# Optimization experiments

Measured on AMD Instinct MI355X. Metric: run time of the kernel, lower is better.

## Reference

```python
import jax, jax.numpy as jnp
import numpy as np

SPLINE_ORDER = 3
BN_EPS = 1e-5


def make_grid(grid_size, lo=-1.0, hi=1.0):
    # torch KANLinear grid: uniform on [lo,hi] extended by spline_order knots each side
    h = (hi - lo) / grid_size
    return jnp.arange(-SPLINE_ORDER, grid_size + SPLINE_ORDER + 1, dtype=jnp.float32) * h + lo


def b_splines(x, grid, k=SPLINE_ORDER):
    # x: [...], grid: [G+2k+1] -> bases [..., G+k] (Cox-de Boor recursion)
    x = x[..., None]
    bases = ((x >= grid[:-1]) & (x < grid[1:])).astype(x.dtype)
    for j in range(1, k + 1):
        left = (x - grid[: -(j + 1)]) / (grid[j:-1] - grid[: -(j + 1)])
        right = (grid[j + 1:] - x) / (grid[j + 1:] - grid[1:-j])
        bases = left * bases[..., :-1] + right * bases[..., 1:]
    return bases


def extract_patches(x, d):
    # 3x3 dilated sliding windows, stride 1, padding == dilation -> same HxW
    B, C, H, W = x.shape
    xp = jnp.pad(x, ((0, 0), (0, 0), (d, d), (d, d)))
    pats = [xp[:, :, ki * d:ki * d + H, kj * d:kj * d + W]
            for ki in range(3) for kj in range(3)]
    return jnp.stack(pats, axis=-1)  # [B,C,H,W,9] (kh-major, matching torch Unfold)


def batchnorm(x, g, b):
    # training-mode BN (torch default forward): batch statistics, biased variance
    mean = x.mean(axis=(0, 2, 3), keepdims=True)
    var = x.var(axis=(0, 2, 3), keepdims=True)
    return (x - mean) / jnp.sqrt(var + BN_EPS) * g[None, :, None, None] + b[None, :, None, None]


def se_block(x, w1, w2):
    y = x.mean(axis=(2, 3))                                  # [B,C]
    y = jax.nn.sigmoid(jax.nn.relu(y @ w1.T) @ w2.T)         # [B,C]
    return x * y[:, :, None, None]


def kan_conv(x, base_w, spline_w, grid, dilation):
    # one KANLinear(9->1) per (out,in) channel pair, summed over in channels
    p = extract_patches(x, dilation)                          # [B,Ci,H,W,9]
    base = jnp.einsum('bihwk,oik->bohw', jax.nn.silu(p), base_w)
    bs = b_splines(p, grid)                                   # [B,Ci,H,W,9,G+k]
    spl = jnp.einsum('bihwkg,oikg->bohw', bs, spline_w)
    return base + spl


def kan_branch(x, base_w, spline_w, grid, dilation, bn_g, bn_b, se_w1, se_w2):
    y = kan_conv(x, base_w, spline_w, grid, dilation)
    y = jax.nn.relu(batchnorm(y, bn_g, bn_b))
    return se_block(y, se_w1, se_w2)


def setup_inputs() -> dict:
    key = jax.random.key(0)
    ks = jax.random.split(key, 16)
    B, Ci, Co, H, W = 2, 64, 64, 64, 64
    r = Co // 16
    d = {"x": jax.random.normal(ks[0], (B, Ci, H, W), jnp.float32)}
    for i, (bname, G) in enumerate([(6, 3), (12, 6), (18, 9)]):
        kk = jax.random.split(ks[1 + i], 4)
        d[f"base_w{bname}"] = jax.random.normal(kk[0], (Co, Ci, 9), jnp.float32) / np.sqrt(9.0 * Ci)
        d[f"spline_w{bname}"] = jax.random.normal(kk[1], (Co, Ci, 9, G + SPLINE_ORDER), jnp.float32) * (0.1 / np.sqrt(9.0 * Ci))
        d[f"bn{bname}_g"] = jnp.ones((Co,), jnp.float32)
        d[f"bn{bname}_b"] = jnp.zeros((Co,), jnp.float32)
        d[f"se{bname}_w1"] = jax.random.normal(kk[2], (r, Co), jnp.float32) / np.sqrt(Co)
        d[f"se{bname}_w2"] = jax.random.normal(kk[3], (Co, r), jnp.float32) / np.sqrt(r)
    d["gp_conv_w"] = jax.random.normal(ks[4], (Co, Ci), jnp.float32) / np.sqrt(Ci)
    d["gp_conv_b"] = jnp.zeros((Co,), jnp.float32)
    d["gp_bn_g"] = jnp.ones((Co,), jnp.float32)
    d["gp_bn_b"] = jnp.zeros((Co,), jnp.float32)
    d["gp_se_w1"] = jax.random.normal(ks[5], (r, Co), jnp.float32) / np.sqrt(Co)
    d["gp_se_w2"] = jax.random.normal(ks[6], (Co, r), jnp.float32) / np.sqrt(r)
    d["fuse_w"] = jax.random.normal(ks[7], (Co, 4 * Co), jnp.float32) / np.sqrt(4.0 * Co)
    d["fuse_b"] = jnp.zeros((Co,), jnp.float32)
    d["fuse_bn_g"] = jnp.ones((Co,), jnp.float32)
    d["fuse_bn_b"] = jnp.zeros((Co,), jnp.float32)
    return d


def reference(x, base_w6, spline_w6, bn6_g, bn6_b, se6_w1, se6_w2,
              base_w12, spline_w12, bn12_g, bn12_b, se12_w1, se12_w2,
              base_w18, spline_w18, bn18_g, bn18_b, se18_w1, se18_w2,
              gp_conv_w, gp_conv_b, gp_bn_g, gp_bn_b, gp_se_w1, gp_se_w2,
              fuse_w, fuse_b, fuse_bn_g, fuse_bn_b):
    B, Ci, H, W = x.shape
    # global-pool branch: avgpool -> 1x1 conv -> BN -> ReLU -> SE -> bilinear
    # upsample (1x1 source => pure broadcast, align_corners irrelevant)
    gp = x.mean(axis=(2, 3)) @ gp_conv_w.T + gp_conv_b      # [B,Co]
    gp = gp[:, :, None, None]
    gp = jax.nn.relu(batchnorm(gp, gp_bn_g, gp_bn_b))
    gp = se_block(gp, gp_se_w1, gp_se_w2)
    gp = jnp.broadcast_to(gp, (B, gp.shape[1], H, W))
    # KAN dilated branches
    b6 = kan_branch(x, base_w6, spline_w6, make_grid(3), 6, bn6_g, bn6_b, se6_w1, se6_w2)
    b12 = kan_branch(x, base_w12, spline_w12, make_grid(6), 12, bn12_g, bn12_b, se12_w1, se12_w2)
    b18 = kan_branch(x, base_w18, spline_w18, make_grid(9), 18, bn18_g, bn18_b, se18_w1, se18_w2)
    cat = jnp.concatenate([b6, b12, b18, gp], axis=1)        # [B,4Co,H,W]
    out = jnp.einsum('bihw,oi->bohw', cat, fuse_w) + fuse_b[None, :, None, None]
    out = jax.nn.relu(batchnorm(out, fuse_bn_g, fuse_bn_b))
    return out
```

## Files before the change

kernel.cpp:

```cpp
#include <hip/hip_runtime.h>
#include <hip/hip_bf16.h>
#include <math.h>

#define DEV __device__ __forceinline__

static constexpr int HW  = 4096;
static constexpr int POS = 8192;
static constexpr int SLAB = 6 * 64 * 4096;

typedef __attribute__((ext_vector_type(8)))  short short8;
typedef __attribute__((ext_vector_type(16))) float floatx16;
typedef __attribute__((ext_vector_type(4)))  unsigned int uint4v;

template<int G>
DEV void bsplines(float x, float* out ) {
  const float h = 2.0f / (float)G;
  float knot[G + 7];
#pragma unroll
  for (int t = 0; t < G + 7; ++t) knot[t] = -1.0f + (float)(t - 3) * h;
  float bb[G + 6];
#pragma unroll
  for (int t = 0; t < G + 6; ++t) bb[t] = (x >= knot[t] && x < knot[t + 1]) ? 1.0f : 0.0f;
#pragma unroll
  for (int j = 1; j <= 3; ++j) {
    const float inv = (float)G / (2.0f * (float)j);
#pragma unroll
    for (int t = 0; t < G + 6 - j; ++t) {
      float left  = (x - knot[t]) * inv;
      float right = (knot[t + j + 1] - x) * inv;
      bb[t] = left * bb[t] + right * bb[t + 1];
    }
  }
#pragma unroll
  for (int t = 0; t < G + 3; ++t) out[t] = bb[t];
}

DEV float sigmoidf_(float x) { return 1.0f / (1.0f + __expf(-x)); }

DEV float block_reduce_256(float v, float* sb) {
  __syncthreads();
#pragma unroll
  for (int off = 32; off > 0; off >>= 1) v += __shfl_down(v, off, 64);
  int lane = threadIdx.x & 63, wid = threadIdx.x >> 6;
  if (lane == 0) sb[wid] = v;
  __syncthreads();
  return sb[0] + sb[1] + sb[2] + sb[3];
}


template<int CF>
DEV void wprep_body(const float* __restrict__ base_w, const float* __restrict__ spline_w,
                    __hip_bfloat16* __restrict__ Wt, int bid) {
  constexpr int KC = 64 * CF;
  int lin = bid * 256 + threadIdx.x;
  int ic = lin % KC;
  int rest = lin / KC;
  int o = rest & 63, tap = rest >> 6;
  int c = ic % CF, i = ic / CF;
  float v = (c == 0) ? base_w[(o * 64 + i) * 9 + tap]
                     : spline_w[((o * 64 + i) * 9 + tap) * (CF - 1) + (c - 1)];
  int s = ic >> 4, kk = ic & 15, q = kk >> 3, r = kk & 7, hh = o >> 5;
  int l = q * 32 + (o & 31);
  Wt[(size_t)tap * (64 * KC) + s * 1024 + hh * 512 + l * 8 + r] = __float2bfloat16(v);
}

template<int G>
DEV void c0r_body(int ki, const float* __restrict__ sw, float* __restrict__ out,
                  float* shmem ) {
  constexpr int NB = G + 3;
  int o = threadIdx.x & 63, part = threadIdx.x >> 6;
  float b0[NB];
  bsplines<G>(0.0f, b0);
  float s = 0.0f;
  for (int kj = 0; kj < 3; ++kj) {
    int tap = ki * 3 + kj;
    for (int i = part * 16; i < part * 16 + 16; ++i) {
      const float* p = sw + ((size_t)(o * 64 + i) * 9 + tap) * NB;
#pragma unroll
      for (int c = 0; c < NB; ++c) s += p[c] * b0[c];
    }
  }
  shmem[part * 64 + o] = s;
  __syncthreads();
  if (part == 0)
    out[ki * 64 + o] = shmem[o] + shmem[64 + o] + shmem[128 + o] + shmem[192 + o];
}

template<int G, int D>
DEV void features_body(const float* __restrict__ x, __hip_bfloat16* __restrict__ F, int bid,
                       __hip_bfloat16* lds ) {
  constexpr int CF = G + 4;
  constexpr int NB = G + 3;
  constexpr int WP = 64 + 2 * D;
  constexpr int NG = WP / 4;
  constexpr int KC = 64 * CF;
  constexpr int RS = 64 * CF + 16;
  int ws = threadIdx.x & 3, i = threadIdx.x >> 2;
  int wpg = bid % NG;
  int rest = bid / NG;
  int h = rest & 63, b = rest >> 6;
  int wp = wpg * 4 + ws;
  int w = wp - D;
  float xv = (w >= 0 && w < 64) ? x[((size_t)(b * 64 + i) * 64 + h) * 64 + w] : 0.0f;
  float s = xv * sigmoidf_(xv);
  float bas[NB];
  bsplines<G>(xv, bas);
  __hip_bfloat16* dst = lds + ws * RS + i * CF;
  dst[0] = __float2bfloat16(s);
#pragma unroll
  for (int c = 1; c < CF; ++c) dst[c] = __float2bfloat16(bas[c - 1]);
  __syncthreads();
  constexpr int TOTV = 32 * CF;
  uint4v* g = (uint4v*)(F + (size_t)(b * 64 + h) * WP * KC);
  const uint4v* l = (const uint4v*)lds;
  for (int t = threadIdx.x; t < TOTV; t += 256) {
    int sc = t >> 3, r = t & 7, wl = r >> 1, k4 = r & 1;
    g[(size_t)(sc * WP + wpg * 4 + wl) * 2 + k4] = l[wl * (8 * CF + 2) + sc * 2 + k4];
  }
}

__global__ void prepfeat_k(const float* __restrict__ x,
                           __hip_bfloat16* F0, __hip_bfloat16* F1, __hip_bfloat16* F2,
                           const float* bw0, const float* sw0, const float* bw1,
                           const float* sw1, const float* bw2, const float* sw2,
                           __hip_bfloat16* W0, __hip_bfloat16* W1, __hip_bfloat16* W2,
                           float* C0r, const float* fuse_w, float* fwT,
                           float* xm, float* accz ) {
  __shared__ uint4v ldsq[424];
  __shared__ float shmem[256];
  __hip_bfloat16* lds = (__hip_bfloat16*)ldsq;
  int bid = blockIdx.x, tid = threadIdx.x;
  if (bid < 2432)      { features_body<3, 6>(x, F0, bid, lds); return; }
  else if (bid < 5248) { features_body<6, 12>(x, F1, bid - 2432, lds); return; }
  else if (bid < 8448) { features_body<9, 18>(x, F2, bid - 5248, lds); return; }
  int pb = bid - 8448;
  if (pb < 1008)      { wprep_body<7>(bw0, sw0, W0, pb); }
  else if (pb < 2448) { wprep_body<10>(bw1, sw1, W1, pb - 1008); }
  else if (pb < 4320) { wprep_body<13>(bw2, sw2, W2, pb - 2448); }
  else if (pb < 4329) {
    int idx = pb - 4320, br = idx / 3, ki = idx % 3;
    if (br == 0)      c0r_body<3>(ki, sw0, C0r, shmem);
    else if (br == 1) c0r_body<6>(ki, sw1, C0r + 192, shmem);
    else              c0r_body<9>(ki, sw2, C0r + 384, shmem);
  } else if (pb < 4377) {
    int lin = (pb - 4329) * 256 + tid;
    int o = lin & 63, i2 = lin >> 6;
    fwT[i2 * 64 + o] = fuse_w[o * 256 + i2];
  } else if (pb < 4505) {
    int bi = pb - 4377;
    const float* p = x + (size_t)bi * HW;
    float s = 0.0f;
    for (int t = tid; t < HW; t += 256) s += p[t];
    s = block_reduce_256(s, shmem);
    if (tid == 0) xm[bi] = s * (1.0f / HW);
  } else {
    for (int t = tid; t < 896; t += 256) accz[t] = 0.0f;
  }
}

DEV floatx16 mfma_bf16(short8 a, short8 b, floatx16 c) {
  return __builtin_amdgcn_mfma_f32_32x32x16_bf16(a, b, c, 0, 0, 0);
}

template<int CF, int DD>
DEV void conv_dev(int ki, int b, int hp, const short* __restrict__ F,
                  const short* __restrict__ W, const float* __restrict__ C0r,
                  float* __restrict__ ypart, int br, float* __restrict__ red) {
  constexpr int KC = 64 * CF;
  constexpr int WP = 64 + 2 * DD;
  int wid = threadIdx.x >> 6;
  int wv  = wid & 1;
  int kjw = wid >> 1;
  int lane = threadIdx.x & 63;
  int lr = lane & 31, lq = lane >> 5;
  int hs = hp * 2 + wv;
  int h_out = hs - (ki - 1) * DD;
  bool valid = (h_out >= 0 && h_out < 64);
  int h_tgt = valid ? h_out : (h_out < 0 ? h_out + 64 : h_out - 64);
  float* yb = ypart + (size_t)ki * SLAB + ((size_t)((br * 2 + b) * 64 + h_tgt)) * 4096;

  floatx16 acc[2][2];
#pragma unroll
  for (int ot = 0; ot < 2; ++ot)
#pragma unroll
    for (int wh = 0; wh < 2; ++wh)
#pragma unroll
      for (int r = 0; r < 16; ++r) acc[ot][wh][r] = 0.0f;

  if (valid) {
    const short* wl_ = W + (size_t)(ki * 3 + kjw) * (64 * KC) + lane * 8;
    const short* fB  = F + (size_t)(b * 64 + hs) * WP * KC
                         + (kjw * DD + lr) * 16 + lq * 8;
#pragma unroll 4
    for (int s = 0; s < 4 * CF; ++s) {
      short8 a0 = *(const short8*)(wl_ + s * 1024);
      short8 a1 = *(const short8*)(wl_ + s * 1024 + 512);
      short8 b0 = *(const short8*)(fB + s * (WP * 16));
      short8 b1 = *(const short8*)(fB + s * (WP * 16) + 512);
      acc[0][0] = mfma_bf16(a0, b0, acc[0][0]);
      acc[0][1] = mfma_bf16(a0, b1, acc[0][1]);
      acc[1][0] = mfma_bf16(a1, b0, acc[1][0]);
      acc[1][1] = mfma_bf16(a1, b1, acc[1][1]);
    }
  }

  float* slot = red + (size_t)wv * (64 * 65) + lane * 65;
  if (kjw == 2 && valid) {
#pragma unroll
    for (int ot = 0; ot < 2; ++ot)
#pragma unroll
      for (int wh = 0; wh < 2; ++wh)
#pragma unroll
        for (int r = 0; r < 16; ++r) slot[(ot * 2 + wh) * 16 + r] = acc[ot][wh][r];
  }
  __syncthreads();
  if (kjw == 1 && valid) {
#pragma unroll
    for (int ot = 0; ot < 2; ++ot)
#pragma unroll
      for (int wh = 0; wh < 2; ++wh)
#pragma unroll
        for (int r = 0; r < 16; ++r) {
          int idx = (ot * 2 + wh) * 16 + r;
          slot[idx] += acc[ot][wh][r];
        }
  }
  __syncthreads();
  if (kjw != 0) return;

  if (!valid) {
    const float* c0 = C0r + (br * 3 + ki) * 64;
#pragma unroll
    for (int wh = 0; wh < 2; ++wh) {
      int w = wh * 32 + lr;
#pragma unroll
      for (int ot = 0; ot < 2; ++ot)
#pragma unroll
        for (int r = 0; r < 16; ++r) {
          int o = (r & 3) + 8 * (r >> 2) + 4 * lq + 32 * ot;
          yb[(size_t)o * 64 + w] = c0[o];
        }
    }
    return;
  }

#pragma unroll
  for (int ot = 0; ot < 2; ++ot)
#pragma unroll
    for (int wh = 0; wh < 2; ++wh) {
      int w = wh * 32 + lr;
#pragma unroll
      for (int r = 0; r < 16; ++r) {
        int o = (r & 3) + 8 * (r >> 2) + 4 * lq + 32 * ot;
        yb[(size_t)o * 64 + w] = acc[ot][wh][r] + slot[(ot * 2 + wh) * 16 + r];
      }
    }
}

__global__ __launch_bounds__(384) void conv_all_k(
    const short* __restrict__ F0, const short* __restrict__ F1, const short* __restrict__ F2,
    const short* __restrict__ W0, const short* __restrict__ W1, const short* __restrict__ W2,
    const float* __restrict__ C0r, float* __restrict__ ypart) {
  __shared__ float red[2 * 64 * 65];
  int bid = blockIdx.x;
  int e  = bid & 7;
  int t  = bid >> 3;
  int ki = t % 3;
  int m  = (t / 3) * 8 + e;
  int br = m >> 6, b = (m >> 5) & 1, hp = m & 31;
  if (br == 0)      conv_dev<7, 6>(ki, b, hp, F0, W0, C0r, ypart, 0, red);
  else if (br == 1) conv_dev<10, 12>(ki, b, hp, F1, W1, C0r, ypart, 1, red);
  else              conv_dev<13, 18>(ki, b, hp, F2, W2, C0r, ypart, 2, red);
}

__global__ void rb_k(float* __restrict__ yp, float* __restrict__ bnacc_s,
                     float* __restrict__ bnacc_q) {
  int bid = blockIdx.x;
  int bb = bid / 256, chunk = bid % 256;
  int br = bb >> 1;
  int tid = threadIdx.x;
  size_t base = (size_t)bb * 262144 + chunk * 1024 + tid * 4;
  float4 v = *(const float4*)(yp + base);
#pragma unroll
  for (int s2 = 1; s2 < 3; ++s2) {
    float4 u = *(const float4*)(yp + base + (size_t)s2 * SLAB);
    v.x += u.x; v.y += u.y; v.z += u.z; v.w += u.w;
  }
  *(float4*)(yp + base) = v;
  float s = v.x + v.y + v.z + v.w;
  float q = v.x * v.x + v.y * v.y + v.z * v.z + v.w * v.w;
  s += __shfl_down(s, 8, 16); s += __shfl_down(s, 4, 16);
  s += __shfl_down(s, 2, 16); s += __shfl_down(s, 1, 16);
  q += __shfl_down(q, 8, 16); q += __shfl_down(q, 4, 16);
  q += __shfl_down(q, 2, 16); q += __shfl_down(q, 1, 16);
  if ((tid & 15) == 0) {
    int o = (chunk * 16 + (tid >> 4)) & 63;
    atomicAdd(&bnacc_s[br * 64 + o], s);
    atomicAdd(&bnacc_q[br * 64 + o], q);
  }
}

__global__ void sesum_k(const float* __restrict__ y, const float* __restrict__ bnacc_s,
                        const float* __restrict__ bnacc_q,
                        const float* g0, const float* b0p, const float* g1, const float* b1p,
                        const float* g2, const float* b2p, float* __restrict__ se_acc) {
  int bid = blockIdx.x;
  int bb = bid >> 6, h = bid & 63;
  int br = bb >> 1;
  int tid = threadIdx.x;
  int o = tid >> 2, wq = tid & 3;
  const float* gptr = (br == 0) ? g0 : ((br == 1) ? g1 : g2);
  const float* bptr = (br == 0) ? b0p : ((br == 1) ? b1p : b2p);
  float mu = bnacc_s[br * 64 + o] * (1.0f / POS);
  float var = bnacc_q[br * 64 + o] * (1.0f / POS) - mu * mu;
  float kk = gptr[o] / sqrtf(var + 1e-5f);
  float cc = bptr[o] - mu * kk;
  const float* row = y + (size_t)bb * 262144 + (size_t)h * 4096 + o * 64 + wq * 16;
  float s = 0.0f;
#pragma unroll
  for (int j = 0; j < 4; ++j) {
    float4 v = *(const float4*)(row + j * 4);
    float a;
    a = v.x * kk + cc; s += (a > 0.0f) ? a : 0.0f;
    a = v.y * kk + cc; s += (a > 0.0f) ? a : 0.0f;
    a = v.z * kk + cc; s += (a > 0.0f) ? a : 0.0f;
    a = v.w * kk + cc; s += (a > 0.0f) ? a : 0.0f;
  }
  s += __shfl_down(s, 2, 4);
  s += __shfl_down(s, 1, 4);
  if (wq == 0) atomicAdd(&se_acc[bb * 64 + o], s);
}

__global__ void semlp_gp_k(const float* __restrict__ se_acc,
                           const float* __restrict__ bnacc_s, const float* __restrict__ bnacc_q,
                           const float* g0, const float* b0p, const float* g1, const float* b1p,
                           const float* g2, const float* b2p,
                           const float* w10, const float* w11, const float* w12,
                           const float* w20, const float* w21, const float* w22,
                           float* __restrict__ A1, float* __restrict__ A0,
                           const float* __restrict__ xm, const float* __restrict__ gw,
                           const float* __restrict__ gb, const float* __restrict__ bng,
                           const float* __restrict__ bnb, const float* __restrict__ gpw1,
                           const float* __restrict__ gpw2, const float* __restrict__ fuse_w,
                           float* __restrict__ fuse_gp) {
  __shared__ float sm[64];
  __shared__ float g0s[2][64], gp1s[2][64], gpvs[2][64];
  int tid = threadIdx.x;
  if (blockIdx.x < 6) {
    int bb = blockIdx.x, br = bb >> 1;
    const float* w1 = (br == 0) ? w10 : ((br == 1) ? w11 : w12);
    const float* w2 = (br == 0) ? w20 : ((br == 1) ? w21 : w22);
    const float* gptr = (br == 0) ? g0 : ((br == 1) ? g1 : g2);
    const float* bptr = (br == 0) ? b0p : ((br == 1) ? b1p : b2p);
    if (tid < 64) sm[tid] = se_acc[bb * 64 + tid] * (1.0f / HW);
    __syncthreads();
    if (tid < 64) {
      int o = tid;
      float z[4];
#pragma unroll
      for (int j = 0; j < 4; ++j) {
        float s = 0.0f;
        for (int c2 = 0; c2 < 64; ++c2) s += sm[c2] * w1[j * 64 + c2];
        z[j] = (s > 0.0f) ? s : 0.0f;
      }
      float t = 0.0f;
#pragma unroll
      for (int j = 0; j < 4; ++j) t += z[j] * w2[o * 4 + j];
      t = sigmoidf_(t);
      float mu = bnacc_s[br * 64 + o] * (1.0f / POS);
      float var = bnacc_q[br * 64 + o] * (1.0f / POS) - mu * mu;
      float kk = gptr[o] / sqrtf(var + 1e-5f);
      float cc = bptr[o] - mu * kk;
      A1[bb * 64 + o] = kk * t;
      A0[bb * 64 + o] = cc * t;
    }
  } else {
    int b = tid >> 6, o = tid & 63;
    float gv = gb[o];
    for (int i = 0; i < 64; ++i) gv += xm[b * 64 + i] * gw[o * 64 + i];
    g0s[b][o] = gv;
    __syncthreads();
    float mu = 0.5f * (g0s[0][o] + g0s[1][o]);
    float df = g0s[0][o] - g0s[1][o];
    float var = 0.25f * df * df;
    float v = (gv - mu) / sqrtf(var + 1e-5f) * bng[o] + bnb[o];
    v = (v > 0.0f) ? v : 0.0f;
    gp1s[b][o] = v;
    __syncthreads();
    float z[4];
#pragma unroll
    for (int j = 0; j < 4; ++j) {
      float s = 0.0f;
      for (int c2 = 0; c2 < 64; ++c2) s += gp1s[b][c2] * gpw1[j * 64 + c2];
      z[j] = (s > 0.0f) ? s : 0.0f;
    }
    float t = 0.0f;
#pragma unroll
    for (int j = 0; j < 4; ++j) t += z[j] * gpw2[o * 4 + j];
    t = sigmoidf_(t);
    gpvs[b][o] = v * t;
    __syncthreads();
    float fg = 0.0f;
    for (int c2 = 0; c2 < 64; ++c2) fg += fuse_w[o * 256 + 192 + c2] * gpvs[b][c2];
    fuse_gp[b * 64 + o] = fg;
  }
}

__global__ __launch_bounds__(256) void fuse_k(
    const float* __restrict__ y, const float* __restrict__ A1, const float* __restrict__ A0,
    const float* __restrict__ fwT, const float* __restrict__ fb, const float* __restrict__ fgp,
    float* __restrict__ tmp, float* __restrict__ fstat) {
  int bid = blockIdx.x;
  int b = bid >> 7, h = (bid >> 1) & 63, wh = bid & 1;
  int tid = threadIdx.x;
  int wg = tid & 7, og = tid >> 3;
  int w0 = wg * 4, o0 = og * 2;
  float acc[2][4] = {};
  __shared__ float As[64][32];
  __shared__ float Ws[64][64];
  for (int br = 0; br < 3; ++br) {
#pragma unroll
    for (int m = 0; m < 8; ++m) {
      int lin = tid + m * 256;
      int oc = lin >> 5, wl = lin & 31;
      float v = y[(size_t)(br * 2 + b) * 262144 + (size_t)h * 4096 + oc * 64 + wh * 32 + wl];
      float a1 = A1[(br * 2 + b) * 64 + oc], a0 = A0[(br * 2 + b) * 64 + oc];
      v = v * a1 + a0;
      As[oc][wl] = (v > 0.0f) ? v : 0.0f;
    }
#pragma unroll
    for (int m = 0; m < 16; ++m) {
      int lin = tid + m * 256;
      int oc = lin >> 6, ol = lin & 63;
      Ws[oc][ol] = fwT[(br * 64 + oc) * 64 + ol];
    }
    __syncthreads();
#pragma unroll 8
    for (int ict = 0; ict < 64; ++ict) {
      float4 a = *reinterpret_cast<const float4*>(&As[ict][w0]);
      float2 wv = *reinterpret_cast<const float2*>(&Ws[ict][o0]);
      acc[0][0] += wv.x * a.x; acc[0][1] += wv.x * a.y; acc[0][2] += wv.x * a.z; acc[0][3] += wv.x * a.w;
      acc[1][0] += wv.y * a.x; acc[1][1] += wv.y * a.y; acc[1][2] += wv.y * a.z; acc[1][3] += wv.y * a.w;
    }
    __syncthreads();
  }
  float* tp = tmp + (size_t)(b * 64 + h) * 4096 + wh * 32;
  float ps[2], pq[2];
#pragma unroll
  for (int oo = 0; oo < 2; ++oo) {
    int o = o0 + oo;
    float bias = fb[o] + fgp[b * 64 + o];
    float4 v = make_float4(acc[oo][0] + bias, acc[oo][1] + bias,
                           acc[oo][2] + bias, acc[oo][3] + bias);
    *reinterpret_cast<float4*>(&tp[o * 64 + w0]) = v;
    ps[oo] = v.x + v.y + v.z + v.w;
    pq[oo] = v.x * v.x + v.y * v.y + v.z * v.z + v.w * v.w;
  }
  __syncthreads();
#pragma unroll
  for (int oo = 0; oo < 2; ++oo) { As[o0 + oo][wg] = ps[oo]; Ws[o0 + oo][wg] = pq[oo]; }
  __syncthreads();
  if (tid < 64) {
    float s = 0.0f, q = 0.0f;
#pragma unroll
    for (int r = 0; r < 8; ++r) { s += As[tid][r]; q += Ws[tid][r]; }
    atomicAdd(&fstat[tid], s);
    atomicAdd(&fstat[64 + tid], q);
  }
}

__global__ void final_k(const float* __restrict__ tmp, const float* __restrict__ fstat,
                        const float* __restrict__ g, const float* __restrict__ bb,
                        float* __restrict__ out) {
  int lin = blockIdx.x * 256 + threadIdx.x;
  int w = lin & 63, h2 = (lin >> 6) & 63, o = (lin >> 12) & 63, b = lin >> 18;
  float v = tmp[((size_t)(b * 64 + h2) * 64 + o) * 64 + w];
  float m = fstat[o] * (1.0f / POS);
  float var = fstat[64 + o] * (1.0f / POS) - m * m;
  float kk = g[o] / sqrtf(var + 1e-5f);
  float r = (v - m) * kk + bb[o];
  out[lin] = (r > 0.0f) ? r : 0.0f;
}

extern "C" void kernel_launch(void* const* d_in, const int* in_sizes, int n_in,
                              void* d_out, int out_size, void* d_ws, size_t ws_size,
                              hipStream_t stream) {
  const float* x = (const float*)d_in[0];
  const float* base_w[3]   = {(const float*)d_in[1],  (const float*)d_in[7],  (const float*)d_in[13]};
  const float* spline_w[3] = {(const float*)d_in[2],  (const float*)d_in[8],  (const float*)d_in[14]};
  const float* bn_g[3]     = {(const float*)d_in[3],  (const float*)d_in[9],  (const float*)d_in[15]};
  const float* bn_b[3]     = {(const float*)d_in[4],  (const float*)d_in[10], (const float*)d_in[16]};
  const float* se_w1[3]    = {(const float*)d_in[5],  (const float*)d_in[11], (const float*)d_in[17]};
  const float* se_w2[3]    = {(const float*)d_in[6],  (const float*)d_in[12], (const float*)d_in[18]};
  const float* gp_conv_w = (const float*)d_in[19];
  const float* gp_conv_b = (const float*)d_in[20];
  const float* gp_bn_g   = (const float*)d_in[21];
  const float* gp_bn_b   = (const float*)d_in[22];
  const float* gp_se_w1  = (const float*)d_in[23];
  const float* gp_se_w2  = (const float*)d_in[24];
  const float* fuse_w    = (const float*)d_in[25];
  const float* fuse_b    = (const float*)d_in[26];
  const float* fuse_bn_g = (const float*)d_in[27];
  const float* fuse_bn_b = (const float*)d_in[28];
  float* out = (float*)d_out;

  char* wsp = (char*)d_ws;
  auto alloc = [&](size_t bytes) -> char* {
    char* p = wsp;
    wsp += (bytes + 255) & ~(size_t)255;
    return p;
  };
  __hip_bfloat16* F0 = (__hip_bfloat16*)alloc((size_t)2 * 64 * 76 * 448 * 2);
  __hip_bfloat16* F1 = (__hip_bfloat16*)alloc((size_t)2 * 64 * 88 * 640 * 2);
  __hip_bfloat16* F2 = (__hip_bfloat16*)alloc((size_t)2 * 64 * 100 * 832 * 2);
  __hip_bfloat16* W0 = (__hip_bfloat16*)alloc((size_t)9 * 64 * 448 * 2);
  __hip_bfloat16* W1 = (__hip_bfloat16*)alloc((size_t)9 * 64 * 640 * 2);
  __hip_bfloat16* W2 = (__hip_bfloat16*)alloc((size_t)9 * 64 * 832 * 2);
  float* C0r   = (float*)alloc((size_t)3 * 3 * 64 * 4);
  float* ypart = (float*)alloc((size_t)3 * SLAB * 4);
  float* y     = ypart;
  float* tmp   = ypart + SLAB;
  float* A1  = (float*)alloc(384 * 4);
  float* A0  = (float*)alloc(384 * 4);
  float* xm  = (float*)alloc(128 * 4);
  float* fgp = (float*)alloc(128 * 4);
  float* fwT = (float*)alloc((size_t)12288 * 4);
  float* accz = (float*)alloc(896 * 4);
  float* fstat   = accz;
  float* bnacc_s = accz + 128;
  float* bnacc_q = accz + 320;
  float* se_acc  = accz + 512;

  prepfeat_k<<<12954, 256, 0, stream>>>(x, F0, F1, F2,
                                        base_w[0], spline_w[0], base_w[1], spline_w[1],
                                        base_w[2], spline_w[2], W0, W1, W2, C0r,
                                        fuse_w, fwT, xm, accz);
  conv_all_k<<<576, 384, 0, stream>>>(
      (const short*)F0, (const short*)F1, (const short*)F2,
      (const short*)W0, (const short*)W1, (const short*)W2, C0r, ypart);
  rb_k<<<1536, 256, 0, stream>>>(ypart, bnacc_s, bnacc_q);
  sesum_k<<<384, 256, 0, stream>>>(y, bnacc_s, bnacc_q, bn_g[0], bn_b[0], bn_g[1], bn_b[1],
                                   bn_g[2], bn_b[2], se_acc);
  semlp_gp_k<<<7, 128, 0, stream>>>(se_acc, bnacc_s, bnacc_q, bn_g[0], bn_b[0], bn_g[1], bn_b[1],
                                    bn_g[2], bn_b[2], se_w1[0], se_w1[1], se_w1[2],
                                    se_w2[0], se_w2[1], se_w2[2], A1, A0,
                                    xm, gp_conv_w, gp_conv_b, gp_bn_g, gp_bn_b,
                                    gp_se_w1, gp_se_w2, fuse_w, fgp);
  fuse_k<<<256, 256, 0, stream>>>(y, A1, A0, fwT, fuse_b, fgp, tmp, fstat);
  final_k<<<2048, 256, 0, stream>>>(tmp, fstat, fuse_bn_g, fuse_bn_b, out);
}
```

Measured before the change: 243.7 us.

## Fuse per-branch feature prep into one interior pass with separate constant halo fill

Feature preparation now has each interior block load x once, compute SiLU once, and write B-spline features for all three dilation branches through a larger shared-memory staging buffer. Halo columns, whose input is the zero padding value, are filled by dedicated blocks that compute the constant bases once and broadcast them with wide stores. This removes redundant global loads of x and repeated SiLU work across branches, and cuts the grid from 12954 to 6752 blocks. In exchange each interior block uses more LDS and registers, which may lower occupancy, and the halo index math is more complex.

```diff
diff --git a/kernel.cpp b/kernel.cpp
--- a/kernel.cpp
+++ b/kernel.cpp
@@ -86,36 +86,75 @@
     out[ki * 64 + o] = shmem[o] + shmem[64 + o] + shmem[128 + o] + shmem[192 + o];
 }
 
+template<int G, int RB>
+DEV void feat_stage(float xv, float s, __hip_bfloat16* lds, int ws, int i) {
+  constexpr int CF = G + 4;
+  constexpr int RS = 64 * CF + 16;
+  float bas[G + 3];
+  bsplines<G>(xv, bas);
+  __hip_bfloat16* d = lds + RB + ws * RS + i * CF;
+  d[0] = __float2bfloat16(s);
+#pragma unroll
+  for (int c = 1; c < CF; ++c) d[c] = __float2bfloat16(bas[c - 1]);
+}
+
+template<int CF, int D, int RBu>
+DEV void feat_copy(__hip_bfloat16* __restrict__ F, int b, int h, int wg, const uint4v* l) {
+  constexpr int WP = 64 + 2 * D;
+  constexpr int KC = 64 * CF;
+  uint4v* g = (uint4v*)(F + (size_t)(b * 64 + h) * WP * KC);
+  for (int t = threadIdx.x; t < 32 * CF; t += 256) {
+    int sc = t >> 3, r = t & 7, wl = r >> 1, k4 = r & 1;
+    g[(size_t)(sc * WP + D + wg * 4 + wl) * 2 + k4] = l[RBu + wl * (8 * CF + 2) + sc * 2 + k4];
+  }
+}
+
+DEV void feat_interior(const float* __restrict__ x, __hip_bfloat16* F0, __hip_bfloat16* F1,
+                       __hip_bfloat16* F2, int bid, __hip_bfloat16* lds) {
+  int tid = threadIdx.x;
+  int ws = tid & 3, i = tid >> 2;
+  int wg = bid & 15, h = (bid >> 4) & 63, b = bid >> 10;
+  int w = wg * 4 + ws;
+  float xv = x[((size_t)(b * 64 + i) * 64 + h) * 64 + w];
+  float s = xv * sigmoidf_(xv);
+  feat_stage<3, 0>(xv, s, lds, ws, i);
+  feat_stage<6, 1856>(xv, s, lds, ws, i);
+  feat_stage<9, 4480>(xv, s, lds, ws, i);
+  __syncthreads();
+  const uint4v* l = (const uint4v*)lds;
+  feat_copy<7, 6, 0>(F0, b, h, wg, l);
+  feat_copy<10, 12, 232>(F1, b, h, wg, l);
+  feat_copy<13, 18, 560>(F2, b, h, wg, l);
+}
+
 template<int G, int D>
-DEV void features_body(const float* __restrict__ x, __hip_bfloat16* __restrict__ F, int bid,
-                       __hip_bfloat16* lds ) {
+DEV void halo_body(__hip_bfloat16* __restrict__ F, int bidl, __hip_bfloat16* ldsb) {
   constexpr int CF = G + 4;
-  constexpr int NB = G + 3;
   constexpr int WP = 64 + 2 * D;
-  constexpr int NG = WP / 4;
   constexpr int KC = 64 * CF;
-  constexpr int RS = 64 * CF + 16;
-  int ws = threadIdx.x & 3, i = threadIdx.x >> 2;
-  int wpg = bid % NG;
-  int rest = bid / NG;
-  int h = rest & 63, b = rest >> 6;
-  int wp = wpg * 4 + ws;
-  int w = wp - D;
-  float xv = (w >= 0 && w < 64) ? x[((size_t)(b * 64 + i) * 64 + h) * 64 + w] : 0.0f;
-  float s = xv * sigmoidf_(xv);
-  float bas[NB];
-  bsplines<G>(xv, bas);
-  __hip_bfloat16* dst = lds + ws * RS + i * CF;
-  dst[0] = __float2bfloat16(s);
-#pragma unroll
-  for (int c = 1; c < CF; ++c) dst[c] = __float2bfloat16(bas[c - 1]);
-  __syncthreads();
-  constexpr int TOTV = 32 * CF;
-  uint4v* g = (uint4v*)(F + (size_t)(b * 64 + h) * WP * KC);
-  const uint4v* l = (const uint4v*)lds;
-  for (int t = threadIdx.x; t < TOTV; t += 256) {
-    int sc = t >> 3, r = t & 7, wl = r >> 1, k4 = r & 1;
-    g[(size_t)(sc * WP + wpg * 4 + wl) * 2 + k4] = l[wl * (8 * CF + 2) + sc * 2 + k4];
+  constexpr int PW = 8 * CF;
+  constexpr int D2 = 2 * D;
+  int tid = threadIdx.x;
+  float bas0[G + 3];
+  bsplines<G>(0.0f, bas0);
+  for (int k = tid; k < KC; k += 256) {
+    int c = k % CF;
+    float v = 0.0f;
+#pragma unroll
+    for (int cc = 1; cc < CF; ++cc) v = (c == cc) ? bas0[cc - 1] : v;
+    ldsb[k] = __float2bfloat16(v);
+  }
+  __syncthreads();
+  const uint4v* l = (const uint4v*)ldsb;
+  uint4v* g = (uint4v*)F;
+#pragma unroll
+  for (int u = 0; u < 16; ++u) {
+    int t = bidl * 4096 + u * 256 + tid;
+    int rw = t / PW, r2 = t - rw * PW;
+    int sc = r2 >> 1, k4 = r2 & 1;
+    int row = rw / D2, wj = rw - row * D2;
+    int wp = (wj < D) ? wj : 64 + wj;
+    g[(size_t)row * (WP * KC / 8) + (size_t)(sc * WP + wp) * 2 + k4] = l[sc * 2 + k4];
   }
 }
 
@@ -126,14 +165,15 @@
                            __hip_bfloat16* W0, __hip_bfloat16* W1, __hip_bfloat16* W2,
                            float* C0r, const float* fuse_w, float* fwT,
                            float* xm, float* accz ) {
-  __shared__ uint4v ldsq[424];
+  __shared__ uint4v ldsq[984];
   __shared__ float shmem[256];
   __hip_bfloat16* lds = (__hip_bfloat16*)ldsq;
   int bid = blockIdx.x, tid = threadIdx.x;
-  if (bid < 2432)      { features_body<3, 6>(x, F0, bid, lds); return; }
-  else if (bid < 5248) { features_body<6, 12>(x, F1, bid - 2432, lds); return; }
-  else if (bid < 8448) { features_body<9, 18>(x, F2, bid - 5248, lds); return; }
-  int pb = bid - 8448;
+  if (bid < 2048)      { feat_interior(x, F0, F1, F2, bid, lds); return; }
+  else if (bid < 2069) { halo_body<3, 6>(F0, bid - 2048, lds); return; }
+  else if (bid < 2129) { halo_body<6, 12>(F1, bid - 2069, lds); return; }
+  else if (bid < 2246) { halo_body<9, 18>(F2, bid - 2129, lds); return; }
+  int pb = bid - 2246;
   if (pb < 1008)      { wprep_body<7>(bw0, sw0, W0, pb); }
   else if (pb < 2448) { wprep_body<10>(bw1, sw1, W1, pb - 1008); }
   else if (pb < 4320) { wprep_body<13>(bw2, sw2, W2, pb - 2448); }
@@ -531,10 +571,10 @@
   float* bnacc_q = accz + 320;
   float* se_acc  = accz + 512;
 
-  prepfeat_k<<<12954, 256, 0, stream>>>(x, F0, F1, F2,
-                                        base_w[0], spline_w[0], base_w[1], spline_w[1],
-                                        base_w[2], spline_w[2], W0, W1, W2, C0r,
-                                        fuse_w, fwT, xm, accz);
+  prepfeat_k<<<6752, 256, 0, stream>>>(x, F0, F1, F2,
+                                       base_w[0], spline_w[0], base_w[1], spline_w[1],
+                                       base_w[2], spline_w[2], W0, W1, W2, C0r,
+                                       fuse_w, fwT, xm, accz);
   conv_all_k<<<576, 384, 0, stream>>>(
       (const short*)F0, (const short*)F1, (const short*)F2,
       (const short*)W0, (const short*)W1, (const short*)W2, C0r, ypart);
```

Result: no change. 243.1 us (-0.2%).
